# Optimization experiments

Measured on AMD Instinct MI355X. Metric: run time of the kernel, lower is better.

The kernel has to match this reference:

```python
import jax, jax.numpy as jnp
import numpy as np

DIM = 768; NH = 8; G = 14; N = G * G + 1; B = 64; PD = DIM // 16; HID = 4 * DIM
SCOPES = (1, 4, 7)


def _build_adj(fs, scope):
    # windowed adjacency on an fs x fs grid, padded with an always-on ACM (class) token
    idx = np.arange(fs)
    ii, jj = np.meshgrid(idx, idx, indexing='ij')
    ri, rj = ii.ravel(), jj.ravel()
    a = ((np.abs(ri[:, None] - ri[None, :]) <= scope) & (np.abs(rj[:, None] - rj[None, :]) <= scope)).astype(np.float32)
    out = np.ones((fs * fs + 1, fs * fs + 1), np.float32)
    out[1:, 1:] = a
    return out


def _prior_adj():
    # loop=0 -> loop1=loop2=0, repeat = NH//4; heads get [adj1,adj1,adj2,adj2,adj3,adj3,ones,ones]
    rep = NH // 4
    mats = [_build_adj(G, s) for s in SCOPES] + [np.ones((N, N), np.float32)]
    return np.stack([m for m in mats for _ in range(rep)], 0)


def _rel_idx():
    coords = np.stack(np.meshgrid(np.arange(G), np.arange(G), indexing='ij')).reshape(2, -1)
    rel = (coords[:, :, None] - coords[:, None, :]).transpose(1, 2, 0).copy()
    rel[..., 0] += G - 1
    rel[..., 1] += G - 1
    rel[..., 0] *= 2 * G - 1
    idx = rel.sum(-1)
    out = np.full((N, N), (2 * G - 1) ** 2 + 1, np.int32)
    out[1:, 1:] = idx
    return out


def _biases():
    r = np.arange(-G, G + 1)  # arange(1-(G+1), G+1)
    g = np.stack(np.meshgrid(r, r, indexing='ij')).reshape(2, -1).T
    return g.astype(np.float32)  # ((2G+1)^2, 2)


def setup_inputs():
    key = jax.random.key(0)
    ks = iter(jax.random.split(key, 32))
    rn = lambda *s: jax.random.normal(next(ks), s, jnp.float32) * 0.02
    return dict(
        x=jax.random.normal(next(ks), (B, N, DIM), jnp.float32),
        norm1_w=jnp.ones(DIM), norm1_b=jnp.zeros(DIM),
        qkv_w=rn(3 * DIM, DIM),
        scale=10.0 * jnp.ones((NH, 1, 1)),
        pp_w=rn(PD, 2), pp_b=jnp.zeros(PD),
        ln1_w=jnp.ones(PD), ln1_b=jnp.zeros(PD), fcp1_w=rn(PD, PD), fcp1_b=jnp.zeros(PD),
        ln2_w=jnp.ones(PD), ln2_b=jnp.zeros(PD), fcp2_w=rn(PD, PD), fcp2_b=jnp.zeros(PD),
        ln3_w=jnp.ones(PD), ln3_b=jnp.zeros(PD), fcp3_w=rn(NH, PD), fcp3_b=jnp.zeros(NH),
        pre_w=rn(NH, NH) + jnp.eye(NH), post_w=rn(NH, NH) + jnp.eye(NH),
        proj_w=rn(DIM, DIM), proj_b=jnp.zeros(DIM),
        norm2_w=jnp.ones(DIM), norm2_b=jnp.zeros(DIM),
        m1_w=rn(HID, DIM), m1_b=jnp.zeros(HID),
        m2_w=rn(DIM, HID), m2_b=jnp.zeros(DIM),
        prior_adj=jnp.asarray(_prior_adj()),
        biases=jnp.asarray(_biases()),
        rel_idx=jnp.asarray(_rel_idx()),
    )


def _ln(x, w, b, eps=1e-5):
    m = x.mean(-1, keepdims=True)
    v = ((x - m) ** 2).mean(-1, keepdims=True)
    return (x - m) / jnp.sqrt(v + eps) * w + b


def _l2n(x, eps=1e-12):
    return x / jnp.maximum(jnp.linalg.norm(x, axis=-1, keepdims=True), eps)


def reference(x, norm1_w, norm1_b, qkv_w, scale, pp_w, pp_b, ln1_w, ln1_b, fcp1_w, fcp1_b, ln2_w, ln2_b, fcp2_w, fcp2_b, ln3_w, ln3_b, fcp3_w, fcp3_b, pre_w, post_w, proj_w, proj_b, norm2_w, norm2_b, m1_w, m1_b, m2_w, m2_b, prior_adj, biases, rel_idx):
    Bq, Nq, C = x.shape
    d = C // NH
    h = _ln(x, norm1_w, norm1_b)
    qkv = (h @ qkv_w.T).reshape(Bq, Nq, 3, NH, d).transpose(2, 0, 3, 1, 4)
    q, k, v = qkv[0], qkv[1], qkv[2]  # each (B, NH, N, d)
    attn = jnp.einsum('bhnd,bhmd->bhnm', _l2n(q), _l2n(k)) * jnp.minimum(scale, 100.0)[None]
    p = biases @ pp_w.T + pp_b
    p = jax.nn.relu(_ln(p, ln1_w, ln1_b)) @ fcp1_w.T + fcp1_b
    p = jax.nn.relu(_ln(p, ln2_w, ln2_b)) @ fcp2_w.T + fcp2_b
    p = jax.nn.relu(_ln(p, ln3_w, ln3_b)) @ fcp3_w.T + fcp3_b  # (841, NH)
    rpb = p[rel_idx]  # (N, N, NH)
    attn = attn + rpb.transpose(2, 0, 1)[None]
    attn = jnp.einsum('oh,bhnm->bonm', pre_w, attn)  # 1x1 conv over heads (pre-softmax)
    attn = jnp.where(prior_adj[None] > 0, attn, -1e9)
    attn = jax.nn.softmax(attn, axis=-1)
    attn = jnp.einsum('oh,bhnm->bonm', post_w, attn)  # 1x1 conv over heads (post-softmax)
    out = jnp.einsum('bhnm,bhmd->bhnd', attn, v).transpose(0, 2, 1, 3).reshape(Bq, Nq, C)
    x = x + (out @ proj_w.T + proj_b)
    h2 = _ln(x, norm2_w, norm2_b)
    h2 = jax.nn.gelu(h2 @ m1_w.T + m1_b, approximate=False) @ m2_w.T + m2_b
    return x + h2
```

## Files before the change

kernel.cpp:

```cpp
#include <hip/hip_runtime.h>
#include <hip/hip_bf16.h>
#include <math.h>

typedef __hip_bfloat16 bf16;
typedef __attribute__((ext_vector_type(8))) short bf16x8;
typedef __attribute__((ext_vector_type(4))) float f32x4;

__device__ __forceinline__ float b2f(bf16 x){ return __bfloat162float(x); }
__device__ __forceinline__ bf16  f2b(float x){ return __float2bfloat16(x); }
__device__ __forceinline__ float us2f(unsigned short u){ bf16 t; *(unsigned short*)&t = u; return __bfloat162float(t); }

__device__ __forceinline__ void gld16(const bf16* g, bf16* l){
    __builtin_amdgcn_global_load_lds(
        (const __attribute__((address_space(1))) unsigned int*)g,
        (__attribute__((address_space(3))) unsigned int*)l, 16, 0, 0);
}

#define NTOK 197
#define NBATCH 64
#define NHEAD 8
#define DHEAD 96
#define DIMC 768
#define NROWS (NBATCH * NTOK)
#define VTS 224
#define SMS 200
#define SBS 224
#define MHALF 6304

#define OFF_P   0ull
#define OFF_W   32768ull
#define SZ_QKVW 3538944ull
#define SZ_PRJW 1179648ull
#define SZ_M1W  4718592ull
#define SZ_M2W  4718592ull
#define OFF_H   14188544ull
#define SZ_H    19365888ull
#define OFF_Q   33554432ull
#define OFF_K   52920320ull
#define OFF_V   72286208ull

__global__ __launch_bounds__(256) void w_cvt_all(
    const float* __restrict__ s0, const float* __restrict__ s1,
    const float* __restrict__ s2, const float* __restrict__ s3, bf16* __restrict__ d)
{
    int i = blockIdx.x*256 + threadIdx.x;
    const float* s; int off;
    if (i < 442368){ s=s0; off=i; }
    else if (i < 589824){ s=s1; off=i-442368; }
    else if (i < 1179648){ s=s2; off=i-589824; }
    else { s=s3; off=i-1179648; }
    float4 v = ((const float4*)s)[off];
    bf16 t[4] = {f2b(v.x), f2b(v.y), f2b(v.z), f2b(v.w)};
    ((ushort4*)d)[i] = *(ushort4*)t;
}

__global__ __launch_bounds__(64) void pos_mlp(
    const float* __restrict__ biases, const float* __restrict__ pp_w, const float* __restrict__ pp_b,
    const float* __restrict__ ln1w, const float* __restrict__ ln1b,
    const float* __restrict__ f1w,  const float* __restrict__ f1b,
    const float* __restrict__ ln2w, const float* __restrict__ ln2b,
    const float* __restrict__ f2w,  const float* __restrict__ f2b,
    const float* __restrict__ ln3w, const float* __restrict__ ln3b,
    const float* __restrict__ f3w,  const float* __restrict__ f3b,
    const float* __restrict__ pre_w,
    float* __restrict__ pout)
{
    const int row = blockIdx.x, j = threadIdx.x;
    __shared__ float va[48], vb[48], pf[8];
    float b0 = biases[row*2], b1 = biases[row*2+1];
    if (j < 48) va[j] = b0*pp_w[j*2] + b1*pp_w[j*2+1] + pp_b[j];
    __syncthreads();
    {   float s=0.f, s2=0.f;
        for (int i=0;i<48;i++){ float t=va[i]; s+=t; s2+=t*t; }
        float mean=s*(1.f/48.f), var=s2*(1.f/48.f)-mean*mean, inv=rsqrtf(var+1e-5f);
        float r=0.f;
        if (j < 48){
            r = f1b[j];
            for (int i=0;i<48;i++){
                float t = fmaxf((va[i]-mean)*inv*ln1w[i] + ln1b[i], 0.f);
                r += t * f1w[j*48+i];
            }
        }
        __syncthreads();
        if (j < 48) vb[j] = r;
    }
    __syncthreads();
    {   float s=0.f, s2=0.f;
        for (int i=0;i<48;i++){ float t=vb[i]; s+=t; s2+=t*t; }
        float mean=s*(1.f/48.f), var=s2*(1.f/48.f)-mean*mean, inv=rsqrtf(var+1e-5f);
        float r=0.f;
        if (j < 48){
            r = f2b[j];
            for (int i=0;i<48;i++){
                float t = fmaxf((vb[i]-mean)*inv*ln2w[i] + ln2b[i], 0.f);
                r += t * f2w[j*48+i];
            }
        }
        __syncthreads();
        if (j < 48) va[j] = r;
    }
    __syncthreads();
    {   float s=0.f, s2=0.f;
        for (int i=0;i<48;i++){ float t=va[i]; s+=t; s2+=t*t; }
        float mean=s*(1.f/48.f), var=s2*(1.f/48.f)-mean*mean, inv=rsqrtf(var+1e-5f);
        if (j < 8){
            float r = f3b[j];
            for (int i=0;i<48;i++){
                float t = fmaxf((va[i]-mean)*inv*ln3w[i] + ln3b[i], 0.f);
                r += t * f3w[j*48+i];
            }
            pf[j] = r;
        }
    }
    __syncthreads();
    if (j < 8){
        float s = 0.f;
        #pragma unroll
        for (int hh=0; hh<8; hh++) s += pre_w[j*8+hh]*pf[hh];
        pout[row*8+j] = s;
    }
}

template<typename TIN>
__global__ __launch_bounds__(256) void ln768(
    const TIN* __restrict__ x, const float* __restrict__ w, const float* __restrict__ b,
    bf16* __restrict__ out)
{
    const int row = blockIdx.x, tid = threadIdx.x;
    const int wv = tid >> 6, ln = tid & 63;
    __shared__ float rs[4], rs2[4];
    const TIN* xr = x + (size_t)row * DIMC;
    float v[4] = {0.f,0.f,0.f,0.f};
    if (tid < 192){
        if constexpr (sizeof(TIN) == 4){
            float4 t4 = ((const float4*)xr)[tid];
            v[0]=t4.x; v[1]=t4.y; v[2]=t4.z; v[3]=t4.w;
        } else {
            ushort4 t4 = ((const ushort4*)xr)[tid];
            v[0]=us2f(t4.x); v[1]=us2f(t4.y); v[2]=us2f(t4.z); v[3]=us2f(t4.w);
        }
    }
    float s = v[0]+v[1]+v[2]+v[3];
    float s2 = v[0]*v[0]+v[1]*v[1]+v[2]*v[2]+v[3]*v[3];
    #pragma unroll
    for (int off=32; off; off>>=1){ s += __shfl_xor(s,off,64); s2 += __shfl_xor(s2,off,64); }
    if (ln == 0){ rs[wv]=s; rs2[wv]=s2; }
    __syncthreads();
    s = rs[0]+rs[1]+rs[2]+rs[3]; s2 = rs2[0]+rs2[1]+rs2[2]+rs2[3];
    float mean = s*(1.f/768.f), var = s2*(1.f/768.f) - mean*mean;
    float inv = rsqrtf(var + 1e-5f);
    if (tid < 192){
        float4 w4 = ((const float4*)w)[tid];
        float4 b4 = ((const float4*)b)[tid];
        bf16 o[4];
        o[0] = f2b((v[0]-mean)*inv*w4.x + b4.x);
        o[1] = f2b((v[1]-mean)*inv*w4.y + b4.y);
        o[2] = f2b((v[2]-mean)*inv*w4.z + b4.z);
        o[3] = f2b((v[3]-mean)*inv*w4.w + b4.w);
        ((ushort4*)(out + (size_t)row*DIMC))[tid] = *(ushort4*)o;
    }
}

__global__ __launch_bounds__(256) void l2norm_qk(bf16* __restrict__ q, bf16* __restrict__ k,
                                                 const float* __restrict__ scale)
{
    const int wv = threadIdx.x >> 6, ln = threadIdx.x & 63;
    const int g = ln >> 4, j = ln & 15;
    const size_t NR = (size_t)NBATCH*NHEAD*NTOK;
    size_t row = (size_t)blockIdx.x*16 + wv*4 + g;
    bool isq = row < NR;
    bf16* ptr = isq ? (q + row*DHEAD) : (k + (row-NR)*DHEAD);
    float xv[8];
    float ss = 0.f;
    if (j < 12){
        bf16x8 vv = *(const bf16x8*)(ptr + j*8);
        #pragma unroll
        for (int e=0;e<8;e++){ float f = us2f((unsigned short)vv[e]); xv[e]=f; ss += f*f; }
    }
    #pragma unroll
    for (int off=8; off; off>>=1) ss += __shfl_xor(ss, off, 64);
    float inv = 1.f / fmaxf(sqrtf(ss), 1e-12f);
    if (isq){
        int h = (int)((row / NTOK) & (NHEAD-1));
        inv *= fminf(scale[h], 100.f);
    }
    if (j < 12){
        bf16x8 ov;
        #pragma unroll
        for (int e=0;e<8;e++){ bf16 t = f2b(xv[e]*inv); ov[e] = *(short*)&t; }
        *(bf16x8*)(ptr + j*8) = ov;
    }
}

__global__ __launch_bounds__(512) void attn_mfma(
    const bf16* __restrict__ q, const bf16* __restrict__ k, const bf16* __restrict__ vt,
    const float* __restrict__ p,
    const float* __restrict__ pre_w, const float* __restrict__ post_w,
    bf16* __restrict__ ao)
{
    const int id = blockIdx.x;
    const int r8 = id & 7, t8 = id >> 3;
    const int bx = t8 % 25, b = r8 + 8*(t8/25);
    const int n0 = bx*8;
    const int tid = threadIdx.x, wv = tid>>6, ln = tid&63;
    const int fr = ln&15, fq = ln>>4;
    __shared__ float S[NHEAD*8*SMS];
    __shared__ float s_pre[64], s_post[64];
    bf16* Sb = (bf16*)S;
    if (tid < 64){ s_pre[tid]=pre_w[tid]; s_post[tid]=post_w[tid]; }

    {
        const int h = wv;
        int qr = n0 + fr; if (qr > 196) qr = 196;
        const bf16* qrow = q + ((size_t)(b*NHEAD+h)*NTOK + qr)*DHEAD + fq*8;
        bf16x8 a0 = *(const bf16x8*)(qrow);
        bf16x8 a1 = *(const bf16x8*)(qrow+32);
        bf16x8 a2 = *(const bf16x8*)(qrow+64);
        const bf16* kb0 = k + (size_t)(b*NHEAD+h)*NTOK*DHEAD + fq*8;
        auto krow = [&](int mt){ int nr = mt*16+fr; if (nr>196) nr=196; return kb0 + (size_t)nr*DHEAD; };
        const bf16* kp0 = krow(0);
        bf16x8 c00 = *(const bf16x8*)(kp0), c01 = *(const bf16x8*)(kp0+32), c02 = *(const bf16x8*)(kp0+64);
        const bf16* kp1 = krow(1);
        bf16x8 c10 = *(const bf16x8*)(kp1), c11 = *(const bf16x8*)(kp1+32), c12 = *(const bf16x8*)(kp1+64);
        #pragma unroll
        for (int mt=0; mt<13; mt++){
            bf16x8 p0, p1, p2;
            if (mt < 11){
                const bf16* kn = krow(mt+2);
                p0 = *(const bf16x8*)(kn); p1 = *(const bf16x8*)(kn+32); p2 = *(const bf16x8*)(kn+64);
            }
            f32x4 acc = {};
            acc = __builtin_amdgcn_mfma_f32_16x16x32_bf16(a0, c00, acc,0,0,0);
            acc = __builtin_amdgcn_mfma_f32_16x16x32_bf16(a1, c01, acc,0,0,0);
            acc = __builtin_amdgcn_mfma_f32_16x16x32_bf16(a2, c02, acc,0,0,0);
            int col = mt*16 + fr;
            if (fq < 2 && col < SMS){
                #pragma unroll
                for (int i=0;i<4;i++)
                    S[(h*8 + fq*4+i)*SMS + col] = acc[i];
            }
            c00=c10; c01=c11; c02=c12;
            if (mt < 11){ c10=p0; c11=p1; c12=p2; }
        }
    }
    __syncthreads();

    if (tid < 256){
        const int sco[8] = {1,1,4,4,7,7,1000,1000};
        const int nq = tid >> 5, l32 = tid & 31;
        int n = n0 + nq; if (n > 196) n = 196;
        const bool nAlways = (n == 0);
        int ri=0, ci=0;
        if (!nAlways){ ri=(n-1)/14; ci=(n-1)-ri*14; }
        for (int m = l32; m < SMS; m += 32){
            if (m >= 197){
                #pragma unroll
                for (int o=0;o<8;o++) S[(o*8+nq)*SMS+m] = -1e9f;
                continue;
            }
            bool always = nAlways || (m==0);
            int rj=0, cj=0;
            if (m > 0){ rj=(m-1)/14; cj=(m-1)-rj*14; }
            int dr = ri-rj; if (dr<0) dr=-dr;
            int dc = ci-cj; if (dc<0) dc=-dc;
            int idx = always ? 730 : (ri-rj+13)*27 + (ci-cj+13);
            const float* pv = p + idx*8;
            float sh[8];
            #pragma unroll
            for (int h2=0;h2<8;h2++) sh[h2] = S[(h2*8+nq)*SMS+m];
            float ov[8];
            #pragma unroll
            for (int o=0;o<8;o++){
                float v = pv[o];
                #pragma unroll
                for (int h2=0;h2<8;h2++) v += s_pre[o*8+h2]*sh[h2];
                bool on = always || (dr<=sco[o] && dc<=sco[o]);
                ov[o] = on ? v : -1e9f;
            }
            #pragma unroll
            for (int o=0;o<8;o++) S[(o*8+nq)*SMS+m] = ov[o];
        }
    }
    __syncthreads();

    {
        const int g = ln >> 4, l16 = ln & 15;
        #pragma unroll
        for (int rr=0; rr<2; rr++){
            float* row = &S[(wv*8 + rr*4 + g)*SMS];
            float mx = -3e38f;
            for (int m=l16; m<SMS; m+=16) mx = fmaxf(mx, row[m]);
            #pragma unroll
            for (int off=8; off; off>>=1) mx = fmaxf(mx, __shfl_xor(mx,off,64));
            float sum = 0.f;
            for (int m=l16; m<SMS; m+=16){ float e=__expf(row[m]-mx); row[m]=e; sum+=e; }
            #pragma unroll
            for (int off=8; off; off>>=1) sum += __shfl_xor(sum,off,64);
            float inv = 1.f/sum;
            for (int m=l16; m<SMS; m+=16) row[m] *= inv;
        }
    }
    __syncthreads();

    {
        const int nq = (tid >> 5) & 7, l32 = tid & 31;
        float ov[7][8];
        if (tid < 256){
            #pragma unroll
            for (int kk=0; kk<7; kk++){
                int m = l32 + 32*kk;
                if (m < 197){
                    float ph[8];
                    #pragma unroll
                    for (int o=0;o<8;o++) ph[o] = S[(o*8+nq)*SMS+m];
                    #pragma unroll
                    for (int o2=0;o2<8;o2++){
                        float v=0.f;
                        #pragma unroll
                        for (int o=0;o<8;o++) v += s_post[o2*8+o]*ph[o];
                        ov[kk][o2]=v;
                    }
                }
            }
        }
        __syncthreads();
        if (tid < 256){
            #pragma unroll
            for (int kk=0; kk<7; kk++){
                int m = l32 + 32*kk;
                #pragma unroll
                for (int o=0;o<8;o++)
                    Sb[(o*8+nq)*SBS + m] = (m < 197) ? f2b(ov[kk][o]) : f2b(0.f);
            }
        }
    }
    __syncthreads();

    {
        const int frA = fr & 7;
        const int h = wv;
        const bf16* vbase = vt + (size_t)(b*NHEAD+h)*DHEAD*VTS;
        bf16x8 pa[7];
        #pragma unroll
        for (int ks=0; ks<7; ks++)
            pa[ks] = *(const bf16x8*)(Sb + (h*8+frA)*SBS + ks*32 + fq*8);
        bf16x8 bv[7], bn[7];
        #pragma unroll
        for (int ks=0; ks<7; ks++)
            bv[ks] = *(const bf16x8*)(vbase + (size_t)fr*VTS + ks*32 + fq*8);
        #pragma unroll
        for (int dt=0; dt<6; dt++){
            if (dt < 5){
                #pragma unroll
                for (int ks=0; ks<7; ks++)
                    bn[ks] = *(const bf16x8*)(vbase + (size_t)((dt+1)*16+fr)*VTS + ks*32 + fq*8);
            }
            f32x4 acc = {};
            #pragma unroll
            for (int ks=0; ks<7; ks++)
                acc = __builtin_amdgcn_mfma_f32_16x16x32_bf16(pa[ks], bv[ks], acc,0,0,0);
            #pragma unroll
            for (int i=0;i<4;i++){
                int nqq = fq*4+i, n = n0+nqq;
                if (nqq < 8 && n < NTOK)
                    ao[((size_t)b*NTOK+n)*DIMC + h*DHEAD + dt*16+fr] = f2b(acc[i]);
            }
            #pragma unroll
            for (int ks=0; ks<7; ks++) bv[ks] = bn[ks];
        }
    }
}

enum { EPI_QKV=0, EPI_X1=1, EPI_GELU=2, EPI_OUT=3 };

template<int EPI>
__global__ __launch_bounds__(256) void gemm128(
    const bf16* __restrict__ A, int lda, int M,
    const bf16* __restrict__ B, int ldb,
    int K,
    const float* __restrict__ bias,
    const float* __restrict__ resid_f,
    const bf16* __restrict__ resid_b,
    float* __restrict__ dst_f,
    bf16* __restrict__ dst_b, int lddb,
    int row_off,
    bf16* __restrict__ qo, bf16* __restrict__ ko, bf16* __restrict__ vto,
    int nbx)
{
    __shared__ bf16 As[2*128*32];
    __shared__ bf16 Bs[2*128*32];
    const int tid = threadIdx.x;
    const int wv = tid >> 6, ln = tid & 63;
    const int fr = ln & 15, fq = ln >> 4;
    const int wr = (wv & 1)*64, wc = (wv >> 1)*64;
    const int nwgs = (int)gridDim.x;
    const int xcd = blockIdx.x & 7;
    const int qq = nwgs >> 3, rr = nwgs & 7;
    const int wg = (xcd < rr ? xcd*(qq+1) : rr*(qq+1) + (xcd-rr)*qq) + ((int)blockIdx.x >> 3);
    const int byi = wg / nbx, bxi = wg - byi*nbx;
    const int m0 = byi*128, n0 = bxi*128;
    const int lnrow = ln >> 2, lncol = (ln & 3)*8;
    f32x4 acc[4][4] = {};
    for (int k0=0; k0<K; k0+=64){
        #pragma unroll
        for (int t=0;t<2;t++){
            #pragma unroll
            for (int c=0;c<2;c++){
                int rA = m0 + (c*4+wv)*16 + lnrow;
                if (rA >= M) rA = M-1;
                gld16(A + (size_t)rA*lda + k0 + t*32 + lncol, &As[t*4096 + (c*4+wv)*16*32]);
                int rB = n0 + (c*4+wv)*16 + lnrow;
                gld16(B + (size_t)rB*ldb + k0 + t*32 + lncol, &Bs[t*4096 + (c*4+wv)*16*32]);
            }
        }
        __syncthreads();
        #pragma unroll
        for (int t=0;t<2;t++){
            bf16x8 af[4], bfv[4];
            #pragma unroll
            for (int i=0;i<4;i++){
                af[i]  = *(const bf16x8*)&As[t*4096 + (wr + i*16 + fr)*32 + fq*8];
                bfv[i] = *(const bf16x8*)&Bs[t*4096 + (wc + i*16 + fr)*32 + fq*8];
            }
            #pragma unroll
            for (int mi=0;mi<4;mi++)
                #pragma unroll
                for (int ni=0;ni<4;ni++)
                    acc[mi][ni] = __builtin_amdgcn_mfma_f32_16x16x32_bf16(af[mi], bfv[ni], acc[mi][ni],0,0,0);
        }
        __syncthreads();
    }
    #pragma unroll
    for (int mi=0;mi<4;mi++){
        #pragma unroll
        for (int ni=0;ni<4;ni++){
            #pragma unroll
            for (int i=0;i<4;i++){
                int row = m0 + wr + mi*16 + fq*4 + i;
                int col = n0 + wc + ni*16 + fr;
                if (row >= M) continue;
                float val = acc[mi][ni][i];
                if constexpr (EPI == EPI_QKV){
                    int which = col/768, rem = col - which*768;
                    int hh = rem/96, di = rem - hh*96;
                    int bb = row/NTOK, nn = row - bb*NTOK;
                    if (which == 0)      qo[(((size_t)bb*NHEAD+hh)*NTOK+nn)*DHEAD + di] = f2b(val);
                    else if (which == 1) ko[(((size_t)bb*NHEAD+hh)*NTOK+nn)*DHEAD + di] = f2b(val);
                    else {
                        vto[(((size_t)bb*NHEAD+hh)*DHEAD+di)*VTS + nn] = f2b(val);
                        if (nn < VTS - NTOK)
                            vto[(((size_t)bb*NHEAD+hh)*DHEAD+di)*VTS + NTOK + nn] = f2b(0.f);
                    }
                } else if constexpr (EPI == EPI_X1){
                    dst_b[(size_t)row*DIMC + col] = f2b(val + bias[col] + resid_f[(size_t)row*DIMC + col]);
                } else if constexpr (EPI == EPI_GELU){
                    float t = val + bias[col];
                    t = 0.5f*t*(1.f + erff(t*0.70710678118654752f));
                    dst_b[(size_t)row*lddb + col] = f2b(t);
                } else {
                    size_t g = (size_t)(row + row_off)*DIMC + col;
                    dst_f[g] = val + bias[col] + b2f(resid_b[g]);
                }
            }
        }
    }
}

extern "C" void kernel_launch(void* const* d_in, const int* in_sizes, int n_in,
                              void* d_out, int out_size, void* d_ws, size_t ws_size,
                              hipStream_t stream)
{
    const float* x        = (const float*)d_in[0];
    const float* norm1_w  = (const float*)d_in[1];
    const float* norm1_b  = (const float*)d_in[2];
    const float* qkv_w    = (const float*)d_in[3];
    const float* scale    = (const float*)d_in[4];
    const float* pp_w     = (const float*)d_in[5];
    const float* pp_b     = (const float*)d_in[6];
    const float* ln1_w    = (const float*)d_in[7];
    const float* ln1_b    = (const float*)d_in[8];
    const float* fcp1_w   = (const float*)d_in[9];
    const float* fcp1_b   = (const float*)d_in[10];
    const float* ln2_w    = (const float*)d_in[11];
    const float* ln2_b    = (const float*)d_in[12];
    const float* fcp2_w   = (const float*)d_in[13];
    const float* fcp2_b   = (const float*)d_in[14];
    const float* ln3_w    = (const float*)d_in[15];
    const float* ln3_b    = (const float*)d_in[16];
    const float* fcp3_w   = (const float*)d_in[17];
    const float* fcp3_b   = (const float*)d_in[18];
    const float* pre_w    = (const float*)d_in[19];
    const float* post_w   = (const float*)d_in[20];
    const float* proj_w   = (const float*)d_in[21];
    const float* proj_b   = (const float*)d_in[22];
    const float* nrm2_w   = (const float*)d_in[23];
    const float* nrm2_b   = (const float*)d_in[24];
    const float* m1_w     = (const float*)d_in[25];
    const float* m1_b     = (const float*)d_in[26];
    const float* m2_w     = (const float*)d_in[27];
    const float* m2_b     = (const float*)d_in[28];
    const float* biases   = (const float*)d_in[30];
    float* out = (float*)d_out;

    char* ws = (char*)d_ws;
    float* p      = (float*)(ws + OFF_P);
    bf16*  qkvw_b = (bf16*)(ws + OFF_W);
    bf16*  prjw_b = (bf16*)(ws + OFF_W + SZ_QKVW);
    bf16*  m1w_b  = (bf16*)(ws + OFF_W + SZ_QKVW + SZ_PRJW);
    bf16*  m2w_b  = (bf16*)(ws + OFF_W + SZ_QKVW + SZ_PRJW + SZ_M1W);
    bf16*  h   = (bf16*)(ws + OFF_H);
    bf16*  qb  = (bf16*)(ws + OFF_Q);
    bf16*  kb  = (bf16*)(ws + OFF_K);
    bf16*  vt  = (bf16*)(ws + OFF_V);
    bf16*  ao  = (bf16*)(ws + OFF_H);
    bf16*  x1b = (bf16*)(ws + OFF_V);
    bf16*  h2  = (bf16*)(ws + OFF_K);
    bf16*  mid = (bf16*)(ws + OFF_H);

    w_cvt_all<<<6912, 256, 0, stream>>>(qkv_w, proj_w, m1_w, m2_w, qkvw_b);
    pos_mlp<<<841, 64, 0, stream>>>(biases, pp_w, pp_b, ln1_w, ln1_b, fcp1_w, fcp1_b,
                                    ln2_w, ln2_b, fcp2_w, fcp2_b, ln3_w, ln3_b, fcp3_w, fcp3_b,
                                    pre_w, p);
    ln768<float><<<NROWS, 256, 0, stream>>>(x, norm1_w, norm1_b, h);
    gemm128<EPI_QKV><<<18*99, 256, 0, stream>>>(
        h, DIMC, NROWS, qkvw_b, DIMC, DIMC, nullptr, nullptr, nullptr, nullptr,
        nullptr, 0, 0, qb, kb, vt, 18);
    l2norm_qk<<<(NBATCH*NHEAD*NTOK*2)/16, 256, 0, stream>>>(qb, kb, scale);
    attn_mfma<<<1600, 512, 0, stream>>>(qb, kb, vt, p, pre_w, post_w, ao);
    gemm128<EPI_X1><<<6*99, 256, 0, stream>>>(
        ao, DIMC, NROWS, prjw_b, DIMC, DIMC, proj_b, x, nullptr, nullptr,
        x1b, 0, 0, nullptr, nullptr, nullptr, 6);
    ln768<bf16><<<NROWS, 256, 0, stream>>>(x1b, nrm2_w, nrm2_b, h2);
    for (int c=0; c<2; c++){
        const int r0 = c*MHALF;
        gemm128<EPI_GELU><<<24*50, 256, 0, stream>>>(
            h2 + (size_t)r0*DIMC, DIMC, MHALF, m1w_b, DIMC, DIMC, m1_b,
            nullptr, nullptr, nullptr, mid, 3072, 0, nullptr, nullptr, nullptr, 24);
        gemm128<EPI_OUT><<<6*50, 256, 0, stream>>>(
            mid, 3072, MHALF, m2w_b, 3072, 3072, m2_b,
            nullptr, x1b, out, nullptr, 0, r0, nullptr, nullptr, nullptr, 6);
    }
    (void)in_sizes; (void)n_in; (void)out_size; (void)ws_size;
}
```

Before: 780.7 us.

## Fuse Q/K L2-normalization into attention kernel and halve its block size

Removes the separate l2norm_qk pass over Q and K. The attention kernel now normalizes Q rows, with the clamped scale, and K tiles in registers right before the MFMA. The attention block shrinks from 512 to 256 threads, and each wave now processes two heads in a loop. This saves a full read-modify-write of Q and K in global memory. The cost is that K is renormalized redundantly by every query block (25 per batch-head), and each thread does twice as much work.

After: 768.5 us. Within noise of the previous version (-1.6%).

```diff
diff --git a/kernel.cpp b/kernel.cpp
--- a/kernel.cpp
+++ b/kernel.cpp
@@ -14,6 +14,27 @@
     __builtin_amdgcn_global_load_lds(
         (const __attribute__((address_space(1))) unsigned int*)g,
         (__attribute__((address_space(3))) unsigned int*)l, 16, 0, 0);
+}
+
+__device__ __forceinline__ void norm3(bf16x8& x0, bf16x8& x1, bf16x8& x2, float extra){
+    float v[24];
+    #pragma unroll
+    for (int e=0;e<8;e++){
+        v[e]    = us2f((unsigned short)x0[e]);
+        v[8+e]  = us2f((unsigned short)x1[e]);
+        v[16+e] = us2f((unsigned short)x2[e]);
+    }
+    float ss = 0.f;
+    #pragma unroll
+    for (int e=0;e<24;e++) ss += v[e]*v[e];
+    ss += __shfl_xor(ss, 16, 64);
+    ss += __shfl_xor(ss, 32, 64);
+    float inv = extra / fmaxf(sqrtf(ss), 1e-12f);
+    #pragma unroll
+    for (int e=0;e<8;e++){
+        bf16 t0=f2b(v[e]*inv), t1=f2b(v[8+e]*inv), t2=f2b(v[16+e]*inv);
+        x0[e]=*(short*)&t0; x1[e]=*(short*)&t1; x2[e]=*(short*)&t2;
+    }
 }
 
 #define NTOK 197
@@ -161,40 +182,10 @@
     }
 }
 
-__global__ __launch_bounds__(256) void l2norm_qk(bf16* __restrict__ q, bf16* __restrict__ k,
-                                                 const float* __restrict__ scale)
-{
-    const int wv = threadIdx.x >> 6, ln = threadIdx.x & 63;
-    const int g = ln >> 4, j = ln & 15;
-    const size_t NR = (size_t)NBATCH*NHEAD*NTOK;
-    size_t row = (size_t)blockIdx.x*16 + wv*4 + g;
-    bool isq = row < NR;
-    bf16* ptr = isq ? (q + row*DHEAD) : (k + (row-NR)*DHEAD);
-    float xv[8];
-    float ss = 0.f;
-    if (j < 12){
-        bf16x8 vv = *(const bf16x8*)(ptr + j*8);
-        #pragma unroll
-        for (int e=0;e<8;e++){ float f = us2f((unsigned short)vv[e]); xv[e]=f; ss += f*f; }
-    }
-    #pragma unroll
-    for (int off=8; off; off>>=1) ss += __shfl_xor(ss, off, 64);
-    float inv = 1.f / fmaxf(sqrtf(ss), 1e-12f);
-    if (isq){
-        int h = (int)((row / NTOK) & (NHEAD-1));
-        inv *= fminf(scale[h], 100.f);
-    }
-    if (j < 12){
-        bf16x8 ov;
-        #pragma unroll
-        for (int e=0;e<8;e++){ bf16 t = f2b(xv[e]*inv); ov[e] = *(short*)&t; }
-        *(bf16x8*)(ptr + j*8) = ov;
-    }
-}
-
-__global__ __launch_bounds__(512) void attn_mfma(
+__global__ __launch_bounds__(256) void attn_mfma(
     const bf16* __restrict__ q, const bf16* __restrict__ k, const bf16* __restrict__ vt,
     const float* __restrict__ p,
+    const float* __restrict__ scale,
     const float* __restrict__ pre_w, const float* __restrict__ post_w,
     bf16* __restrict__ ao)
 {
@@ -209,13 +200,15 @@
     bf16* Sb = (bf16*)S;
     if (tid < 64){ s_pre[tid]=pre_w[tid]; s_post[tid]=post_w[tid]; }
 
-    {
-        const int h = wv;
+    #pragma unroll
+    for (int hh=0; hh<2; hh++){
+        const int h = wv + hh*4;
         int qr = n0 + fr; if (qr > 196) qr = 196;
         const bf16* qrow = q + ((size_t)(b*NHEAD+h)*NTOK + qr)*DHEAD + fq*8;
         bf16x8 a0 = *(const bf16x8*)(qrow);
         bf16x8 a1 = *(const bf16x8*)(qrow+32);
         bf16x8 a2 = *(const bf16x8*)(qrow+64);
+        norm3(a0, a1, a2, fminf(scale[h], 100.f));
         const bf16* kb0 = k + (size_t)(b*NHEAD+h)*NTOK*DHEAD + fq*8;
         auto krow = [&](int mt){ int nr = mt*16+fr; if (nr>196) nr=196; return kb0 + (size_t)nr*DHEAD; };
         const bf16* kp0 = krow(0);
@@ -229,10 +222,12 @@
                 const bf16* kn = krow(mt+2);
                 p0 = *(const bf16x8*)(kn); p1 = *(const bf16x8*)(kn+32); p2 = *(const bf16x8*)(kn+64);
             }
+            bf16x8 k0 = c00, k1 = c01, k2 = c02;
+            norm3(k0, k1, k2, 1.f);
             f32x4 acc = {};
-            acc = __builtin_amdgcn_mfma_f32_16x16x32_bf16(a0, c00, acc,0,0,0);
-            acc = __builtin_amdgcn_mfma_f32_16x16x32_bf16(a1, c01, acc,0,0,0);
-            acc = __builtin_amdgcn_mfma_f32_16x16x32_bf16(a2, c02, acc,0,0,0);
+            acc = __builtin_amdgcn_mfma_f32_16x16x32_bf16(a0, k0, acc,0,0,0);
+            acc = __builtin_amdgcn_mfma_f32_16x16x32_bf16(a1, k1, acc,0,0,0);
+            acc = __builtin_amdgcn_mfma_f32_16x16x32_bf16(a2, k2, acc,0,0,0);
             int col = mt*16 + fr;
             if (fq < 2 && col < SMS){
                 #pragma unroll
@@ -245,7 +240,7 @@
     }
     __syncthreads();
 
-    if (tid < 256){
+    {
         const int sco[8] = {1,1,4,4,7,7,1000,1000};
         const int nq = tid >> 5, l32 = tid & 31;
         int n = n0 + nq; if (n > 196) n = 196;
@@ -286,8 +281,8 @@
     {
         const int g = ln >> 4, l16 = ln & 15;
         #pragma unroll
-        for (int rr=0; rr<2; rr++){
-            float* row = &S[(wv*8 + rr*4 + g)*SMS];
+        for (int rr=0; rr<4; rr++){
+            float* row = &S[(wv*16 + rr*4 + g)*SMS];
             float mx = -3e38f;
             for (int m=l16; m<SMS; m+=16) mx = fmaxf(mx, row[m]);
             #pragma unroll
@@ -303,42 +298,39 @@
     __syncthreads();
 
     {
-        const int nq = (tid >> 5) & 7, l32 = tid & 31;
+        const int nq = tid >> 5, l32 = tid & 31;
         float ov[7][8];
-        if (tid < 256){
-            #pragma unroll
-            for (int kk=0; kk<7; kk++){
-                int m = l32 + 32*kk;
-                if (m < 197){
-                    float ph[8];
+        #pragma unroll
+        for (int kk=0; kk<7; kk++){
+            int m = l32 + 32*kk;
+            if (m < 197){
+                float ph[8];
+                #pragma unroll
+                for (int o=0;o<8;o++) ph[o] = S[(o*8+nq)*SMS+m];
+                #pragma unroll
+                for (int o2=0;o2<8;o2++){
+                    float v=0.f;
                     #pragma unroll
-                    for (int o=0;o<8;o++) ph[o] = S[(o*8+nq)*SMS+m];
-                    #pragma unroll
-                    for (int o2=0;o2<8;o2++){
-                        float v=0.f;
-                        #pragma unroll
-                        for (int o=0;o<8;o++) v += s_post[o2*8+o]*ph[o];
-                        ov[kk][o2]=v;
-                    }
+                    for (int o=0;o<8;o++) v += s_post[o2*8+o]*ph[o];
+                    ov[kk][o2]=v;
                 }
             }
         }
         __syncthreads();
-        if (tid < 256){
-            #pragma unroll
-            for (int kk=0; kk<7; kk++){
-                int m = l32 + 32*kk;
-                #pragma unroll
-                for (int o=0;o<8;o++)
-                    Sb[(o*8+nq)*SBS + m] = (m < 197) ? f2b(ov[kk][o]) : f2b(0.f);
-            }
-        }
-    }
-    __syncthreads();
-
-    {
-        const int frA = fr & 7;
-        const int h = wv;
+        #pragma unroll
+        for (int kk=0; kk<7; kk++){
+            int m = l32 + 32*kk;
+            #pragma unroll
+            for (int o=0;o<8;o++)
+                Sb[(o*8+nq)*SBS + m] = (m < 197) ? f2b(ov[kk][o]) : f2b(0.f);
+        }
+    }
+    __syncthreads();
+
+    const int frA = fr & 7;
+    #pragma unroll
+    for (int hh=0; hh<2; hh++){
+        const int h = wv + hh*4;
         const bf16* vbase = vt + (size_t)(b*NHEAD+h)*DHEAD*VTS;
         bf16x8 pa[7];
         #pragma unroll
@@ -525,8 +517,7 @@
     gemm128<EPI_QKV><<<18*99, 256, 0, stream>>>(
         h, DIMC, NROWS, qkvw_b, DIMC, DIMC, nullptr, nullptr, nullptr, nullptr,
         nullptr, 0, 0, qb, kb, vt, 18);
-    l2norm_qk<<<(NBATCH*NHEAD*NTOK*2)/16, 256, 0, stream>>>(qb, kb, scale);
-    attn_mfma<<<1600, 512, 0, stream>>>(qb, kb, vt, p, pre_w, post_w, ao);
+    attn_mfma<<<1600, 256, 0, stream>>>(qb, kb, vt, p, scale, pre_w, post_w, ao);
     gemm128<EPI_X1><<<6*99, 256, 0, stream>>>(
         ao, DIMC, NROWS, prjw_b, DIMC, DIMC, proj_b, x, nullptr, nullptr,
         x1b, 0, 0, nullptr, nullptr, nullptr, 6);
```

## Apply q/k L2 norms as per-row scales in attention; halve attention block size

Applied to the files above, without the earlier changes.

The q/k normalization kernel now only computes per-row inverse norms (with the clamped scale folded into q) into a float buffer instead of rewriting q and k in place. The attention kernel scales the raw QK^T logits by the q and k inverse norms, which removes a full read-modify-write pass over q and k. The attention block also drops from 512 to 256 threads, with each wave handling two heads in the QK and PV phases and all threads joining the softmax and head-mix stages. This may raise occupancy, at the cost of more serial work per wave and slightly different rounding, since normalization now happens after the bf16 dot product.

Result: no change. 765.6 us (-1.9%).

```diff
diff --git a/kernel.cpp b/kernel.cpp
--- a/kernel.cpp
+++ b/kernel.cpp
@@ -22,6 +22,7 @@
 #define DHEAD 96
 #define DIMC 768
 #define NROWS (NBATCH * NTOK)
+#define NQK   (NBATCH*NHEAD*NTOK)
 #define VTS 224
 #define SMS 200
 #define SBS 224
@@ -38,6 +39,7 @@
 #define OFF_Q   33554432ull
 #define OFF_K   52920320ull
 #define OFF_V   72286208ull
+#define OFF_NRM 94306304ull
 
 __global__ __launch_bounds__(256) void w_cvt_all(
     const float* __restrict__ s0, const float* __restrict__ s1,
@@ -161,40 +163,38 @@
     }
 }
 
-__global__ __launch_bounds__(256) void l2norm_qk(bf16* __restrict__ q, bf16* __restrict__ k,
-                                                 const float* __restrict__ scale)
+__global__ __launch_bounds__(256) void qknorm(
+    const bf16* __restrict__ q, const bf16* __restrict__ k,
+    const float* __restrict__ scale, float* __restrict__ inv)
 {
     const int wv = threadIdx.x >> 6, ln = threadIdx.x & 63;
     const int g = ln >> 4, j = ln & 15;
-    const size_t NR = (size_t)NBATCH*NHEAD*NTOK;
+    const size_t NR = (size_t)NQK;
     size_t row = (size_t)blockIdx.x*16 + wv*4 + g;
     bool isq = row < NR;
-    bf16* ptr = isq ? (q + row*DHEAD) : (k + (row-NR)*DHEAD);
-    float xv[8];
+    const bf16* ptr = isq ? (q + row*DHEAD) : (k + (row-NR)*DHEAD);
     float ss = 0.f;
     if (j < 12){
         bf16x8 vv = *(const bf16x8*)(ptr + j*8);
         #pragma unroll
-        for (int e=0;e<8;e++){ float f = us2f((unsigned short)vv[e]); xv[e]=f; ss += f*f; }
+        for (int e=0;e<8;e++){ float f = us2f((unsigned short)vv[e]); ss += f*f; }
     }
     #pragma unroll
     for (int off=8; off; off>>=1) ss += __shfl_xor(ss, off, 64);
-    float inv = 1.f / fmaxf(sqrtf(ss), 1e-12f);
-    if (isq){
-        int h = (int)((row / NTOK) & (NHEAD-1));
-        inv *= fminf(scale[h], 100.f);
-    }
-    if (j < 12){
-        bf16x8 ov;
-        #pragma unroll
-        for (int e=0;e<8;e++){ bf16 t = f2b(xv[e]*inv); ov[e] = *(short*)&t; }
-        *(bf16x8*)(ptr + j*8) = ov;
-    }
-}
-
-__global__ __launch_bounds__(512) void attn_mfma(
+    if (j == 0){
+        float iv = 1.f / fmaxf(sqrtf(ss), 1e-12f);
+        if (isq){
+            int h = (int)((row / NTOK) & (NHEAD-1));
+            iv *= fminf(scale[h], 100.f);
+        }
+        inv[row] = iv;
+    }
+}
+
+__global__ __launch_bounds__(256) void attn_mfma(
     const bf16* __restrict__ q, const bf16* __restrict__ k, const bf16* __restrict__ vt,
     const float* __restrict__ p,
+    const float* __restrict__ inv,
     const float* __restrict__ pre_w, const float* __restrict__ post_w,
     bf16* __restrict__ ao)
 {
@@ -209,8 +209,17 @@
     bf16* Sb = (bf16*)S;
     if (tid < 64){ s_pre[tid]=pre_w[tid]; s_post[tid]=post_w[tid]; }
 
-    {
-        const int h = wv;
+    #pragma unroll
+    for (int hh=0; hh<2; hh++){
+        const int h = wv + hh*4;
+        const float* iqh = inv + (size_t)(b*NHEAD+h)*NTOK;
+        const float* ikh = inv + (size_t)NQK + (size_t)(b*NHEAD+h)*NTOK;
+        float iqv[4];
+        #pragma unroll
+        for (int i=0;i<4;i++){
+            int nidx = n0 + fq*4 + i; if (nidx > 196) nidx = 196;
+            iqv[i] = iqh[nidx];
+        }
         int qr = n0 + fr; if (qr > 196) qr = 196;
         const bf16* qrow = q + ((size_t)(b*NHEAD+h)*NTOK + qr)*DHEAD + fq*8;
         bf16x8 a0 = *(const bf16x8*)(qrow);
@@ -224,6 +233,8 @@
         bf16x8 c10 = *(const bf16x8*)(kp1), c11 = *(const bf16x8*)(kp1+32), c12 = *(const bf16x8*)(kp1+64);
         #pragma unroll
         for (int mt=0; mt<13; mt++){
+            int mc = mt*16 + fr; if (mc > 196) mc = 196;
+            float ik = ikh[mc];
             bf16x8 p0, p1, p2;
             if (mt < 11){
                 const bf16* kn = krow(mt+2);
@@ -237,7 +248,7 @@
             if (fq < 2 && col < SMS){
                 #pragma unroll
                 for (int i=0;i<4;i++)
-                    S[(h*8 + fq*4+i)*SMS + col] = acc[i];
+                    S[(h*8 + fq*4+i)*SMS + col] = acc[i]*iqv[i]*ik;
             }
             c00=c10; c01=c11; c02=c12;
             if (mt < 11){ c10=p0; c11=p1; c12=p2; }
@@ -245,7 +256,7 @@
     }
     __syncthreads();
 
-    if (tid < 256){
+    {
         const int sco[8] = {1,1,4,4,7,7,1000,1000};
         const int nq = tid >> 5, l32 = tid & 31;
         int n = n0 + nq; if (n > 196) n = 196;
@@ -286,8 +297,8 @@
     {
         const int g = ln >> 4, l16 = ln & 15;
         #pragma unroll
-        for (int rr=0; rr<2; rr++){
-            float* row = &S[(wv*8 + rr*4 + g)*SMS];
+        for (int rr=0; rr<4; rr++){
+            float* row = &S[(wv*16 + rr*4 + g)*SMS];
             float mx = -3e38f;
             for (int m=l16; m<SMS; m+=16) mx = fmaxf(mx, row[m]);
             #pragma unroll
@@ -296,49 +307,46 @@
             for (int m=l16; m<SMS; m+=16){ float e=__expf(row[m]-mx); row[m]=e; sum+=e; }
             #pragma unroll
             for (int off=8; off; off>>=1) sum += __shfl_xor(sum,off,64);
-            float inv = 1.f/sum;
-            for (int m=l16; m<SMS; m+=16) row[m] *= inv;
+            float inv2 = 1.f/sum;
+            for (int m=l16; m<SMS; m+=16) row[m] *= inv2;
         }
     }
     __syncthreads();
 
     {
-        const int nq = (tid >> 5) & 7, l32 = tid & 31;
+        const int nq = tid >> 5, l32 = tid & 31;
         float ov[7][8];
-        if (tid < 256){
-            #pragma unroll
-            for (int kk=0; kk<7; kk++){
-                int m = l32 + 32*kk;
-                if (m < 197){
-                    float ph[8];
+        #pragma unroll
+        for (int kk=0; kk<7; kk++){
+            int m = l32 + 32*kk;
+            if (m < 197){
+                float ph[8];
+                #pragma unroll
+                for (int o=0;o<8;o++) ph[o] = S[(o*8+nq)*SMS+m];
+                #pragma unroll
+                for (int o2=0;o2<8;o2++){
+                    float v=0.f;
                     #pragma unroll
-                    for (int o=0;o<8;o++) ph[o] = S[(o*8+nq)*SMS+m];
-                    #pragma unroll
-                    for (int o2=0;o2<8;o2++){
-                        float v=0.f;
-                        #pragma unroll
-                        for (int o=0;o<8;o++) v += s_post[o2*8+o]*ph[o];
-                        ov[kk][o2]=v;
-                    }
+                    for (int o=0;o<8;o++) v += s_post[o2*8+o]*ph[o];
+                    ov[kk][o2]=v;
                 }
             }
         }
         __syncthreads();
-        if (tid < 256){
-            #pragma unroll
-            for (int kk=0; kk<7; kk++){
-                int m = l32 + 32*kk;
-                #pragma unroll
-                for (int o=0;o<8;o++)
-                    Sb[(o*8+nq)*SBS + m] = (m < 197) ? f2b(ov[kk][o]) : f2b(0.f);
-            }
-        }
-    }
-    __syncthreads();
-
-    {
-        const int frA = fr & 7;
-        const int h = wv;
+        #pragma unroll
+        for (int kk=0; kk<7; kk++){
+            int m = l32 + 32*kk;
+            #pragma unroll
+            for (int o=0;o<8;o++)
+                Sb[(o*8+nq)*SBS + m] = (m < 197) ? f2b(ov[kk][o]) : f2b(0.f);
+        }
+    }
+    __syncthreads();
+
+    const int frA = fr & 7;
+    #pragma unroll
+    for (int hh=0; hh<2; hh++){
+        const int h = wv + hh*4;
         const bf16* vbase = vt + (size_t)(b*NHEAD+h)*DHEAD*VTS;
         bf16x8 pa[7];
         #pragma unroll
@@ -512,6 +520,7 @@
     bf16*  qb  = (bf16*)(ws + OFF_Q);
     bf16*  kb  = (bf16*)(ws + OFF_K);
     bf16*  vt  = (bf16*)(ws + OFF_V);
+    float* inv = (float*)(ws + OFF_NRM);
     bf16*  ao  = (bf16*)(ws + OFF_H);
     bf16*  x1b = (bf16*)(ws + OFF_V);
     bf16*  h2  = (bf16*)(ws + OFF_K);
@@ -525,8 +534,8 @@
     gemm128<EPI_QKV><<<18*99, 256, 0, stream>>>(
         h, DIMC, NROWS, qkvw_b, DIMC, DIMC, nullptr, nullptr, nullptr, nullptr,
         nullptr, 0, 0, qb, kb, vt, 18);
-    l2norm_qk<<<(NBATCH*NHEAD*NTOK*2)/16, 256, 0, stream>>>(qb, kb, scale);
-    attn_mfma<<<1600, 512, 0, stream>>>(qb, kb, vt, p, pre_w, post_w, ao);
+    qknorm<<<(2*NQK)/16, 256, 0, stream>>>(qb, kb, scale, inv);
+    attn_mfma<<<1600, 256, 0, stream>>>(qb, kb, vt, p, inv, pre_w, post_w, ao);
     gemm128<EPI_X1><<<6*99, 256, 0, stream>>>(
         ao, DIMC, NROWS, prjw_b, DIMC, DIMC, proj_b, x, nullptr, nullptr,
         x1b, 0, 0, nullptr, nullptr, nullptr, 6);
```
